# Kernel tuning notes

Hardware: AMD Instinct MI355X
Metric: run time of the kernel (lower is better)

Reference implementation:

```python
import jax, jax.numpy as jnp
import numpy as np

EMB = 1024
HEADS = 16
S = EMB // HEADS  # 64
B, T = 2, 2048


def setup_inputs() -> dict:
    key = jax.random.key(0)
    ks = jax.random.split(key, 5)
    x = jax.random.normal(ks[0], (B, T, EMB), dtype=jnp.float32)
    Wk = jax.random.normal(ks[1], (S, S), dtype=jnp.float32) * (1.0 / np.sqrt(S))
    Wq = jax.random.normal(ks[2], (S, S), dtype=jnp.float32) * (1.0 / np.sqrt(S))
    Wv = jax.random.normal(ks[3], (S, S), dtype=jnp.float32) * (1.0 / np.sqrt(S))
    Wu = jax.random.normal(ks[4], (EMB, EMB), dtype=jnp.float32) * (1.0 / np.sqrt(EMB))
    bu = jnp.zeros((EMB,), dtype=jnp.float32)
    return {"x": x, "Wk": Wk, "Wq": Wq, "Wv": Wv, "Wu": Wu, "bu": bu}


def reference(x, Wk, Wq, Wv, Wu, bu):
    b, t, e = x.shape
    h, s = HEADS, e // HEADS
    xh = x.reshape(b, t, h, s)
    # torch Linear: y = x @ W.T (per-head projection, weights shared across heads)
    keys = jnp.einsum('bths,os->btho', xh, Wk)
    queries = jnp.einsum('bths,os->btho', xh, Wq)
    values = jnp.einsum('bths,os->btho', xh, Wv)
    scale = e ** (-0.25)
    queries = queries * scale
    keys = keys * scale
    # [b, h, t_q, t_k] full score matrix (as in the original bmm)
    dot = jnp.einsum('bqhd,bkhd->bhqk', queries, keys)
    attn = jax.nn.softmax(dot, axis=-1)
    out = jnp.einsum('bhqk,bkhd->bqhd', attn, values).reshape(b, t, e)
    return out @ Wu.T + bu
```

## Files before the change

### kernel.cpp

```cpp
#include <hip/hip_runtime.h>
#include <hip/hip_bf16.h>
#include <stdint.h>

#define TT   2048
#define EMB  1024
#define SDIM 64
#define KVB  64
#define NIT  (TT / KVB)
#define LOG2E 1.4426950408889634f

typedef float f32x2  __attribute__((ext_vector_type(2)));
typedef float f32x4  __attribute__((ext_vector_type(4)));
typedef float f32x16 __attribute__((ext_vector_type(16)));
typedef short short8 __attribute__((ext_vector_type(8)));
typedef unsigned short ushort4v __attribute__((ext_vector_type(4)));
typedef unsigned int uint2v __attribute__((ext_vector_type(2)));
typedef unsigned int uint4v __attribute__((ext_vector_type(4)));

__device__ __forceinline__ ushort f2bf(float f) {
    uint32_t u = __builtin_bit_cast(uint32_t, f);
    u += 0x7FFFu + ((u >> 16) & 1u);
    return (ushort)(u >> 16);
}

__device__ __forceinline__ short8 cvt8(const float* p) {
    f32x4 a = *(const f32x4*)p;
    f32x4 b = *(const f32x4*)(p + 4);
    short8 r;
    r[0] = (short)f2bf(a[0]); r[1] = (short)f2bf(a[1]);
    r[2] = (short)f2bf(a[2]); r[3] = (short)f2bf(a[3]);
    r[4] = (short)f2bf(b[0]); r[5] = (short)f2bf(b[1]);
    r[6] = (short)f2bf(b[2]); r[7] = (short)f2bf(b[3]);
    return r;
}

__device__ __forceinline__ void gload16(const void* g, void* l) {
    __builtin_amdgcn_global_load_lds((const __attribute__((address_space(1))) uint32_t*)g,
                                     (__attribute__((address_space(3))) uint32_t*)l, 16, 0, 0);
}
__device__ __forceinline__ uint pkbf(float a, float b) {
    uint d; asm("v_cvt_pk_bf16_f32 %0, %1, %2" : "=v"(d) : "v"(a), "v"(b)); return d;
}
__device__ __forceinline__ void swap32(uint& a, uint& b) {
    asm volatile("s_nop 1\n\tv_permlane32_swap_b32 %0, %1" : "+v"(a), "+v"(b));
}
__device__ __forceinline__ float xhadd(float x) {
    uint a = __builtin_bit_cast(uint, x), o;
    asm volatile("v_mov_b32 %0, %1\n\ts_nop 3\n\tv_permlane32_swap_b32 %0, %1"
                 : "=&v"(o), "+v"(a));
    return __builtin_bit_cast(float, o) + __builtin_bit_cast(float, a);
}

__global__ __launch_bounds__(256) void cvt_w(const float* __restrict__ Wk, const float* __restrict__ Wq,
                                             const float* __restrict__ Wv,
                                             ushort* __restrict__ Wk16, ushort* __restrict__ Wq16,
                                             ushort* __restrict__ Wv16) {
    int i = blockIdx.x * 256 + threadIdx.x;
    Wk16[i] = f2bf(Wk[i]);
    Wq16[i] = f2bf(Wq[i] * (0.03125f * LOG2E));
    Wv16[i] = f2bf(Wv[i]);
}

__global__ __launch_bounds__(256) void qkv(const float* __restrict__ x,
                                           const ushort* __restrict__ Wk16, const ushort* __restrict__ Wq16,
                                           const ushort* __restrict__ Wv16,
                                           ushort* __restrict__ Qw, ushort* __restrict__ Kw, ushort* __restrict__ Vt,
                                           const float* __restrict__ Wu, ushort* __restrict__ Wu16) {
    const int tid = threadIdx.x;
    if (blockIdx.x >= 1024) {
        const int gbase = ((blockIdx.x - 1024) * 256 + tid) * 16;
#pragma unroll
        for (int j = 0; j < 4; ++j) {
            f32x4 v = *(const f32x4*)(Wu + gbase + 4 * j);
            ushort4v o;
#pragma unroll
            for (int e = 0; e < 4; ++e) o[e] = f2bf(v[e]);
            *(ushort4v*)(Wu16 + gbase + 4 * j) = o;
        }
        return;
    }
    const int wave = tid >> 6, lane = tid & 63;
    const int c = lane & 15, g = lane >> 4;
    const int rblk = (blockIdx.x * 4 + wave) * 16;
    const int bh = rblk >> 11;
    const int tbase = rblk & (TT - 1);
    const int b = bh >> 4, h = bh & 15;

    const float* xrow = x + ((size_t)(b * TT + tbase + c) * EMB + h * SDIM);
    short8 a[2];
#pragma unroll
    for (int ks = 0; ks < 2; ++ks) a[ks] = cvt8(xrow + 32 * ks + 8 * g);

    f32x4 aq[4], ak[4], av[4];
#pragma unroll
    for (int n = 0; n < 4; ++n) { aq[n] = 0.f; ak[n] = 0.f; av[n] = 0.f; }

#pragma unroll
    for (int n = 0; n < 4; ++n) {
#pragma unroll
        for (int ks = 0; ks < 2; ++ks) {
            const size_t wo = (size_t)(16 * n + c) * SDIM + 32 * ks + 8 * g;
            short8 bq = *(const short8*)(Wq16 + wo);
            short8 bk = *(const short8*)(Wk16 + wo);
            short8 bv = *(const short8*)(Wv16 + wo);
            aq[n] = __builtin_amdgcn_mfma_f32_16x16x32_bf16(a[ks], bq, aq[n], 0, 0, 0);
            ak[n] = __builtin_amdgcn_mfma_f32_16x16x32_bf16(a[ks], bk, ak[n], 0, 0, 0);
            av[n] = __builtin_amdgcn_mfma_f32_16x16x32_bf16(a[ks], bv, av[n], 0, 0, 0);
        }
    }
    const size_t hb = (size_t)bh * TT * SDIM;
#pragma unroll
    for (int n = 0; n < 4; ++n) {
#pragma unroll
        for (int i = 0; i < 4; ++i) {
            const size_t o = hb + (size_t)(tbase + 4 * g + i) * SDIM + 16 * n + c;
            Qw[o] = f2bf(aq[n][i]);
            Kw[o] = f2bf(ak[n][i]);
        }
        ushort4v vp;
#pragma unroll
        for (int i = 0; i < 4; ++i) vp[i] = f2bf(av[n][i]);
        *(ushort4v*)(Vt + hb + (size_t)(16 * n + c) * TT + tbase + 4 * g) = vp;
    }
}

__global__ __launch_bounds__(256, 4) void attn(const ushort* __restrict__ Qw, const ushort* __restrict__ Kw,
                                               const ushort* __restrict__ Vt, ushort* __restrict__ AO) {
    __shared__ ushort smem[4][4096];

    const int tid = threadIdx.x;
    const int wv = tid >> 6, lane = tid & 63;
    const int q = lane & 31, hi = lane >> 5;
    const int qg = wv & 1, kh = wv >> 1;

    const int wg = blockIdx.x;
    const int xcd = wg & 7, slot = wg >> 3;
    const int bh = xcd * 4 + (slot >> 5);
    const int qt = slot & 31;
    const int b = bh >> 4, h = bh & 15;
    const int qrowW = qt * 64 + qg * 32;
    const size_t base = (size_t)bh * TT * SDIM;

    short8 qa[4];
    const ushort* Qp = Qw + base + (size_t)(qrowW + q) * SDIM + 8 * hi;
#pragma unroll
    for (int sb = 0; sb < 4; ++sb) qa[sb] = *(const short8*)(Qp + 16 * sb);

    f32x16 a0v = 0.f, a1v = 0.f;
    float lsum = 0.f;

    const int krow = lane >> 3;
    const ushort* Ks = Kw + base + (size_t)(wv * 8 + krow) * SDIM + (((lane & 7) ^ (krow & 7)) * 8);
    const ushort* Vs = Vt + base + (size_t)(wv * 8 + krow) * TT + (((lane & 7) ^ (krow & 7)) * 8);

#define STAGE(kvb, buf) { \
    char* kb = (char*)&smem[(buf)][0] + wv * 1024;      \
    char* vb = (char*)&smem[2 + (buf)][0] + wv * 1024;  \
    _Pragma("unroll")                                    \
    for (int p = 0; p < 2; ++p) {                        \
        gload16(Ks + (kvb) * 64 + p * 2048, kb + p * 4096); \
        gload16(Vs + (kvb) + p * 32 * TT,   vb + p * 4096); \
    } }

    STAGE(0, 0);
    __syncthreads();

    const int kmask = (q & 7) << 4;
    const int vmask = q & 7;
    int cur = 0;
    for (int kt = 0; kt < NIT; ++kt) {
        if (kt < NIT - 1) STAGE((kt + 1) * KVB, cur ^ 1);
        const char* Kc = (const char*)&smem[cur][0];
        const char* Vc = (const char*)&smem[2 + cur][0];

        f32x16 s0 = 0.f;
        __builtin_amdgcn_s_setprio(1);
#pragma unroll
        for (int sb = 0; sb < 4; ++sb) {
            const int off = (32 * sb + 16 * hi) ^ kmask;
            short8 k0 = *(const short8*)(Kc + (kh * 32 + q) * 128 + off);
            s0 = __builtin_amdgcn_mfma_f32_32x32x16_bf16(k0, qa[sb], s0, 0, 0, 0);
        }
        __builtin_amdgcn_s_setprio(0);

        float r0 = 0.f;
#pragma unroll
        for (int i = 0; i < 16; ++i) { float p = __builtin_amdgcn_exp2f(s0[i]); s0[i] = p; r0 += p; }
        lsum += r0;

        short8 pb0, pb1;
        {
            uint u0 = pkbf(s0[0], s0[1]),   u1 = pkbf(s0[2], s0[3]);
            uint u2 = pkbf(s0[4], s0[5]),   u3 = pkbf(s0[6], s0[7]);
            swap32(u0, u2); swap32(u1, u3);
            uint4v ta = {u0, u1, u2, u3}; pb0 = __builtin_bit_cast(short8, ta);
            uint u4 = pkbf(s0[8], s0[9]),   u5 = pkbf(s0[10], s0[11]);
            uint u6 = pkbf(s0[12], s0[13]), u7 = pkbf(s0[14], s0[15]);
            swap32(u4, u6); swap32(u5, u7);
            uint4v tb = {u4, u5, u6, u7}; pb1 = __builtin_bit_cast(short8, tb);
        }

        __builtin_amdgcn_s_setprio(1);
#pragma unroll
        for (int ks = 0; ks < 2; ++ks) {
            short8 pbk = ks ? pb1 : pb0;
            const int u = ((4 * kh + 2 * ks + hi) ^ vmask) << 4;
            short8 v0 = *(const short8*)(Vc + q * 128 + u);
            a0v = __builtin_amdgcn_mfma_f32_32x32x16_bf16(v0, pbk, a0v, 0, 0, 0);
            short8 v1 = *(const short8*)(Vc + (32 + q) * 128 + u);
            a1v = __builtin_amdgcn_mfma_f32_32x32x16_bf16(v1, pbk, a1v, 0, 0, 0);
        }
        __builtin_amdgcn_s_setprio(0);

        __syncthreads();
        cur ^= 1;
    }
#undef STAGE

    f32x2* ob = (f32x2*)&smem[0][0];
    float* lb = (float*)&smem[0][0] + 4096;
    const int mb = qg * 1024 + lane;
    if (kh) {
#pragma unroll
        for (int j = 0; j < 8; ++j) { f32x2 t = {a0v[2 * j], a0v[2 * j + 1]}; ob[mb + j * 64] = t; }
#pragma unroll
        for (int j = 0; j < 8; ++j) { f32x2 t = {a1v[2 * j], a1v[2 * j + 1]}; ob[mb + (8 + j) * 64] = t; }
        lb[qg * 64 + lane] = lsum;
    }
    __syncthreads();
    if (kh) return;

#pragma unroll
    for (int j = 0; j < 8; ++j) { f32x2 t = ob[mb + j * 64];       a0v[2 * j] += t[0]; a0v[2 * j + 1] += t[1]; }
#pragma unroll
    for (int j = 0; j < 8; ++j) { f32x2 t = ob[mb + (8 + j) * 64]; a1v[2 * j] += t[0]; a1v[2 * j + 1] += t[1]; }
    lsum += lb[qg * 64 + lane];

    const float l_i = xhadd(lsum);
    char* scrB = (char*)&smem[0][0] + 20480 + qg * 4096;
    const int eswz = (q & 7) << 4;
    float inv = 1.f / l_i;
#pragma unroll
    for (int sb2 = 0; sb2 < 2; ++sb2) {
#pragma unroll
        for (int bq = 0; bq < 4; ++bq) {
            float v0 = (sb2 ? a1v[4 * bq + 0] : a0v[4 * bq + 0]) * inv;
            float v1 = (sb2 ? a1v[4 * bq + 1] : a0v[4 * bq + 1]) * inv;
            float v2 = (sb2 ? a1v[4 * bq + 2] : a0v[4 * bq + 2]) * inv;
            float v3 = (sb2 ? a1v[4 * bq + 3] : a0v[4 * bq + 3]) * inv;
            uint2v d; d[0] = pkbf(v0, v1); d[1] = pkbf(v2, v3);
            int s0e = 8 * bq + 4 * hi + 32 * sb2;
            *(uint2v*)(scrB + q * 128 + ((s0e * 2) ^ eswz)) = d;
        }
    }
    asm volatile("s_waitcnt lgkmcnt(0)" ::: "memory");
    ushort* AOp = AO + (size_t)(b * TT + qrowW + q) * EMB + h * SDIM + 32 * hi;
#pragma unroll
    for (int jj = 0; jj < 4; ++jj) {
        short8 o = *(const short8*)(scrB + q * 128 + ((64 * hi + 16 * jj) ^ eswz));
        *(short8*)(AOp + 8 * jj) = o;
    }
}

__global__ __launch_bounds__(512) void oproj(const ushort* __restrict__ AO, const ushort* __restrict__ Wu16,
                                             const float* __restrict__ bu, float* __restrict__ out) {
    __shared__ ushort Ab[2][128 * 64];
    __shared__ ushort Bb[2][128 * 64];
    const int tid = threadIdx.x;
    const int wv = tid >> 6, lane = tid & 63;
    const int c = lane & 15, g = lane >> 4;
    const int wr = wv >> 1, wc = wv & 1;
    const int wg = blockIdx.x;
    const int xcd = wg & 7, i6 = wg >> 3;
    const int rblk = (xcd * 4 + (i6 >> 3)) * 128;
    const int nblk = (i6 & 7) * 128;

    const int row0 = tid >> 3;
    const int col0 = ((tid & 7) ^ (row0 & 7)) * 8;
    const ushort* As0 = AO   + (size_t)(rblk + row0) * EMB + col0;
    const ushort* As1 = AO   + (size_t)(rblk + row0 + 64) * EMB + col0;
    const ushort* Bs0 = Wu16 + (size_t)(nblk + row0) * EMB + col0;
    const ushort* Bs1 = Wu16 + (size_t)(nblk + row0 + 64) * EMB + col0;
    const int l0 = wv * 512, l1 = 4096 + wv * 512;

    f32x4 acc[2][4];
#pragma unroll
    for (int m = 0; m < 2; ++m)
#pragma unroll
        for (int n = 0; n < 4; ++n) acc[m][n] = 0.f;

    gload16(As0, &Ab[0][l0]); gload16(As1, &Ab[0][l1]);
    gload16(Bs0, &Bb[0][l0]); gload16(Bs1, &Bb[0][l1]);
    __syncthreads();

    const int swzA = (c & 7) << 4;
    int cur = 0;
    for (int kt = 0; kt < 16; ++kt) {
        if (kt < 15) {
            const int k0 = (kt + 1) * 64;
            gload16(As0 + k0, &Ab[cur ^ 1][l0]); gload16(As1 + k0, &Ab[cur ^ 1][l1]);
            gload16(Bs0 + k0, &Bb[cur ^ 1][l0]); gload16(Bs1 + k0, &Bb[cur ^ 1][l1]);
        }
        const char* Ac = (const char*)&Ab[cur][0];
        const char* Bc = (const char*)&Bb[cur][0];
#pragma unroll
        for (int kb = 0; kb < 2; ++kb) {
            short8 am[2], bn[4];
#pragma unroll
            for (int m = 0; m < 2; ++m)
                am[m] = *(const short8*)(Ac + (wr * 32 + 16 * m + c) * 128 + ((64 * kb + 16 * g) ^ swzA));
#pragma unroll
            for (int n = 0; n < 4; ++n)
                bn[n] = *(const short8*)(Bc + (wc * 64 + 16 * n + c) * 128 + ((64 * kb + 16 * g) ^ swzA));
#pragma unroll
            for (int m = 0; m < 2; ++m)
#pragma unroll
                for (int n = 0; n < 4; ++n)
                    acc[m][n] = __builtin_amdgcn_mfma_f32_16x16x32_bf16(am[m], bn[n], acc[m][n], 0, 0, 0);
        }
        __syncthreads();
        cur ^= 1;
    }
#pragma unroll
    for (int m = 0; m < 2; ++m)
#pragma unroll
        for (int n = 0; n < 4; ++n) {
            float bias = bu[nblk + wc * 64 + 16 * n + c];
#pragma unroll
            for (int i = 0; i < 4; ++i)
                out[(size_t)(rblk + wr * 32 + 16 * m + 4 * g + i) * EMB + nblk + wc * 64 + 16 * n + c] =
                    acc[m][n][i] + bias;
        }
}

extern "C" void kernel_launch(void* const* d_in, const int* in_sizes, int n_in,
                              void* d_out, int out_size, void* d_ws, size_t ws_size,
                              hipStream_t stream) {
    const float* x  = (const float*)d_in[0];
    const float* Wk = (const float*)d_in[1];
    const float* Wq = (const float*)d_in[2];
    const float* Wv = (const float*)d_in[3];
    const float* Wu = (const float*)d_in[4];
    const float* bu = (const float*)d_in[5];
    float* out = (float*)d_out;

    char* ws = (char*)d_ws;
    const size_t MB = 1024u * 1024u;
    ushort* Qw   = (ushort*)(ws);
    ushort* Kw   = (ushort*)(ws + 8 * MB);
    ushort* Vt   = (ushort*)(ws + 16 * MB);
    ushort* AO   = (ushort*)(ws + 24 * MB);
    ushort* Wu16 = (ushort*)(ws + 32 * MB);
    ushort* Wk16 = (ushort*)(ws + 34 * MB);
    ushort* Wq16 = Wk16 + 4096;
    ushort* Wv16 = Wk16 + 8192;

    cvt_w<<<dim3(16), dim3(256), 0, stream>>>(Wk, Wq, Wv, Wk16, Wq16, Wv16);
    qkv<<<dim3(1280), dim3(256), 0, stream>>>(x, Wk16, Wq16, Wv16, Qw, Kw, Vt, Wu, Wu16);
    attn<<<dim3(1024), dim3(256), 0, stream>>>(Qw, Kw, Vt, AO);
    oproj<<<dim3(256), dim3(512), 0, stream>>>(AO, Wu16, bu, out);
}
```

Measured before the change: 88.80 us.

## Widen attention blocks to 8 waves sharing each staged K/V tile

The attention kernel now launches 512-thread blocks covering 128 query rows (4 query groups × 2 key halves) instead of 256-thread blocks covering 64 rows, halving the grid. Each staged 64-key K/V tile in LDS is therefore reused by twice as many query rows, which halves global/L2 traffic for K and V per query. The staging loads shrink to one 16-byte load per thread per tile, and the shared-memory layout and epilogue scratch are reorganised, adding an extra barrier. The s_setprio hints around the MFMA sections are removed. Larger blocks raise per-block register and LDS pressure and reduce the number of resident blocks, which may hurt latency hiding.

```diff
diff --git a/kernel.cpp b/kernel.cpp
--- a/kernel.cpp
+++ b/kernel.cpp
@@ -124,21 +124,21 @@
     }
 }
 
-__global__ __launch_bounds__(256, 4) void attn(const ushort* __restrict__ Qw, const ushort* __restrict__ Kw,
+__global__ __launch_bounds__(512, 6) void attn(const ushort* __restrict__ Qw, const ushort* __restrict__ Kw,
                                                const ushort* __restrict__ Vt, ushort* __restrict__ AO) {
-    __shared__ ushort smem[4][4096];
+    __shared__ ushort smem[17408];
 
     const int tid = threadIdx.x;
     const int wv = tid >> 6, lane = tid & 63;
     const int q = lane & 31, hi = lane >> 5;
-    const int qg = wv & 1, kh = wv >> 1;
+    const int qg = wv & 3, kh = wv >> 2;
 
     const int wg = blockIdx.x;
     const int xcd = wg & 7, slot = wg >> 3;
-    const int bh = xcd * 4 + (slot >> 5);
-    const int qt = slot & 31;
+    const int bh = xcd * 4 + (slot >> 4);
+    const int qt = slot & 15;
     const int b = bh >> 4, h = bh & 15;
-    const int qrowW = qt * 64 + qg * 32;
+    const int qrowW = qt * 128 + qg * 32;
     const size_t base = (size_t)bh * TT * SDIM;
 
     short8 qa[4];
@@ -149,18 +149,16 @@
     f32x16 a0v = 0.f, a1v = 0.f;
     float lsum = 0.f;
 
-    const int krow = lane >> 3;
-    const ushort* Ks = Kw + base + (size_t)(wv * 8 + krow) * SDIM + (((lane & 7) ^ (krow & 7)) * 8);
-    const ushort* Vs = Vt + base + (size_t)(wv * 8 + krow) * TT + (((lane & 7) ^ (krow & 7)) * 8);
+    const int srow = lane >> 3;
+    const int scol = ((lane & 7) ^ srow) * 8;
+    const ushort* Ks = Kw + base + (size_t)(wv * 8 + srow) * SDIM + scol;
+    const ushort* Vs = Vt + base + (size_t)(wv * 8 + srow) * TT + scol;
 
 #define STAGE(kvb, buf) { \
-    char* kb = (char*)&smem[(buf)][0] + wv * 1024;      \
-    char* vb = (char*)&smem[2 + (buf)][0] + wv * 1024;  \
-    _Pragma("unroll")                                    \
-    for (int p = 0; p < 2; ++p) {                        \
-        gload16(Ks + (kvb) * 64 + p * 2048, kb + p * 4096); \
-        gload16(Vs + (kvb) + p * 32 * TT,   vb + p * 4096); \
-    } }
+    char* kb = (char*)smem + (buf) * 8192 + wv * 1024;          \
+    char* vb = (char*)smem + 16384 + (buf) * 8192 + wv * 1024;  \
+    gload16(Ks + (size_t)(kvb) * 64, kb);                       \
+    gload16(Vs + (kvb), vb); }
 
     STAGE(0, 0);
     __syncthreads();
@@ -170,18 +168,16 @@
     int cur = 0;
     for (int kt = 0; kt < NIT; ++kt) {
         if (kt < NIT - 1) STAGE((kt + 1) * KVB, cur ^ 1);
-        const char* Kc = (const char*)&smem[cur][0];
-        const char* Vc = (const char*)&smem[2 + cur][0];
+        const char* Kc = (const char*)smem + cur * 8192;
+        const char* Vc = (const char*)smem + 16384 + cur * 8192;
 
         f32x16 s0 = 0.f;
-        __builtin_amdgcn_s_setprio(1);
 #pragma unroll
         for (int sb = 0; sb < 4; ++sb) {
             const int off = (32 * sb + 16 * hi) ^ kmask;
             short8 k0 = *(const short8*)(Kc + (kh * 32 + q) * 128 + off);
             s0 = __builtin_amdgcn_mfma_f32_32x32x16_bf16(k0, qa[sb], s0, 0, 0, 0);
         }
-        __builtin_amdgcn_s_setprio(0);
 
         float r0 = 0.f;
 #pragma unroll
@@ -200,7 +196,6 @@
             uint4v tb = {u4, u5, u6, u7}; pb1 = __builtin_bit_cast(short8, tb);
         }
 
-        __builtin_amdgcn_s_setprio(1);
 #pragma unroll
         for (int ks = 0; ks < 2; ++ks) {
             short8 pbk = ks ? pb1 : pb0;
@@ -210,15 +205,14 @@
             short8 v1 = *(const short8*)(Vc + (32 + q) * 128 + u);
             a1v = __builtin_amdgcn_mfma_f32_32x32x16_bf16(v1, pbk, a1v, 0, 0, 0);
         }
-        __builtin_amdgcn_s_setprio(0);
 
         __syncthreads();
         cur ^= 1;
     }
 #undef STAGE
 
-    f32x2* ob = (f32x2*)&smem[0][0];
-    float* lb = (float*)&smem[0][0] + 4096;
+    f32x2* ob = (f32x2*)smem;
+    float* lb = (float*)((char*)smem + 32768);
     const int mb = qg * 1024 + lane;
     if (kh) {
 #pragma unroll
@@ -228,16 +222,18 @@
         lb[qg * 64 + lane] = lsum;
     }
     __syncthreads();
+    if (!kh) {
+#pragma unroll
+        for (int j = 0; j < 8; ++j) { f32x2 t = ob[mb + j * 64];       a0v[2 * j] += t[0]; a0v[2 * j + 1] += t[1]; }
+#pragma unroll
+        for (int j = 0; j < 8; ++j) { f32x2 t = ob[mb + (8 + j) * 64]; a1v[2 * j] += t[0]; a1v[2 * j + 1] += t[1]; }
+        lsum += lb[qg * 64 + lane];
+    }
+    __syncthreads();
     if (kh) return;
 
-#pragma unroll
-    for (int j = 0; j < 8; ++j) { f32x2 t = ob[mb + j * 64];       a0v[2 * j] += t[0]; a0v[2 * j + 1] += t[1]; }
-#pragma unroll
-    for (int j = 0; j < 8; ++j) { f32x2 t = ob[mb + (8 + j) * 64]; a1v[2 * j] += t[0]; a1v[2 * j + 1] += t[1]; }
-    lsum += lb[qg * 64 + lane];
-
     const float l_i = xhadd(lsum);
-    char* scrB = (char*)&smem[0][0] + 20480 + qg * 4096;
+    char* scrB = (char*)smem + qg * 4096;
     const int eswz = (q & 7) << 4;
     float inv = 1.f / l_i;
 #pragma unroll
@@ -357,6 +353,6 @@
 
     cvt_w<<<dim3(16), dim3(256), 0, stream>>>(Wk, Wq, Wv, Wk16, Wq16, Wv16);
     qkv<<<dim3(1280), dim3(256), 0, stream>>>(x, Wk16, Wq16, Wv16, Qw, Kw, Vt, Wu, Wu16);
-    attn<<<dim3(1024), dim3(256), 0, stream>>>(Qw, Kw, Vt, AO);
+    attn<<<dim3(512), dim3(512), 0, stream>>>(Qw, Kw, Vt, AO);
     oproj<<<dim3(256), dim3(512), 0, stream>>>(AO, Wu16, bu, out);
 }
```

After: 101.5 us. 14.4% more time.
